# Kernel tuning notes

Measured on AMD Instinct MI355X. Metric: run time of the kernel, lower is better.

The kernel has to match this reference:

```python
import jax, jax.numpy as jnp
import numpy as np
from jax import lax


def _lstm_cell(x, h, c, W_ih, W_hh, b_ih, b_hh):
    # PyTorch LSTMCell math, gate order: input, forget, cell(g), output
    gates = x @ W_ih.T + h @ W_hh.T + b_ih + b_hh  # [B, 4H]
    i, f, g, o = jnp.split(gates, 4, axis=-1)
    i = jax.nn.sigmoid(i)
    f = jax.nn.sigmoid(f)
    g = jnp.tanh(g)
    o = jax.nn.sigmoid(o)
    c_new = f * c + i * g
    h_new = o * jnp.tanh(c_new)
    return h_new, c_new


def setup_inputs() -> dict:
    key = jax.random.key(0)
    ks = jax.random.split(key, 9)
    T, B, D, H = 512, 64, 512, 1024
    s = 0.02  # small init scale to keep recurrence stable
    return {
        "inputs": jax.random.normal(ks[0], (T, B, D), dtype=jnp.float32),
        "W_ih0": jax.random.normal(ks[1], (4 * H, D), dtype=jnp.float32) * s,
        "W_hh0": jax.random.normal(ks[2], (4 * H, H), dtype=jnp.float32) * s,
        "b_ih0": jax.random.normal(ks[3], (4 * H,), dtype=jnp.float32) * s,
        "b_hh0": jax.random.normal(ks[4], (4 * H,), dtype=jnp.float32) * s,
        "W_ih1": jax.random.normal(ks[5], (4 * H, H), dtype=jnp.float32) * s,
        "W_hh1": jax.random.normal(ks[6], (4 * H, H), dtype=jnp.float32) * s,
        "b_ih1": jax.random.normal(ks[7], (4 * H,), dtype=jnp.float32) * s,
        "b_hh1": jax.random.normal(ks[8], (4 * H,), dtype=jnp.float32) * s,
    }


def reference(inputs, W_ih0, W_hh0, b_ih0, b_hh0, W_ih1, W_hh1, b_ih1, b_hh1):
    # 2-layer LSTM over time via lax.scan; dropout=0.0, residual=False.
    T, B, _ = inputs.shape
    H = W_hh0.shape[1]
    z = jnp.zeros((B, H), dtype=inputs.dtype)
    init = (z, z, z, z)  # (h0, c0, h1, c1)

    def step(carry, x_t):
        h0, c0, h1, c1 = carry
        h0, c0 = _lstm_cell(x_t, h0, c0, W_ih0, W_hh0, b_ih0, b_hh0)
        h1, c1 = _lstm_cell(h0, h1, c1, W_ih1, W_hh1, b_ih1, b_hh1)
        return (h0, c0, h1, c1), h1

    (h0, c0, h1, c1), outputs = lax.scan(step, init, inputs)
    # outputs: [T, B, H] from last layer; final states per layer
    return outputs, (h0, c0, h1, c1)
```

## Files before the change

### kernel.cpp

```cpp
#include <hip/hip_runtime.h>
#include <hip/hip_bf16.h>
#include <stdint.h>


#define T_STEPS 512
#define BATCH   64
#define DIN     512
#define HID     1024
#define NBLK    256
#define NTHR    512

typedef __attribute__((ext_vector_type(8)))  short short8;
typedef __attribute__((ext_vector_type(16))) float f32x16;

union U16 { unsigned long long u[2]; short8 v; };

#define OFF_WIH0 ((size_t)0)
#define OFF_WHH0 ((size_t)4194304)
#define OFF_WIH1 ((size_t)12582912)
#define OFF_WHH1 ((size_t)20971520)
#define OFF_XBF  ((size_t)29360128)
#define OFF_H0   ((size_t)62914560)
#define OFF_H1   ((size_t)(OFF_H0 + 262144))
#define OFF_FLG  ((size_t)(OFF_H1 + 262144))

__global__ void cvt_bf16x4(const float4* __restrict__ in,
                           ushort4* __restrict__ out, int n4) {
  int i = blockIdx.x * blockDim.x + threadIdx.x;
  if (i >= n4) return;
  float4 v = in[i];
  __hip_bfloat16 b0 = __float2bfloat16(v.x), b1 = __float2bfloat16(v.y),
                 b2 = __float2bfloat16(v.z), b3 = __float2bfloat16(v.w);
  ushort4 o;
  o.x = *(unsigned short*)&b0; o.y = *(unsigned short*)&b1;
  o.z = *(unsigned short*)&b2; o.w = *(unsigned short*)&b3;
  out[i] = o;
}

__device__ __forceinline__ float sigf(float x) {
  return 1.0f / (1.0f + __expf(-x));
}
__device__ __forceinline__ float tanhfast(float x) {
  return 1.0f - 2.0f / (__expf(2.0f * x) + 1.0f);
}

__launch_bounds__(NTHR, 2)
__global__ void lstm_persist(const __hip_bfloat16* __restrict__ whh0,
                             const __hip_bfloat16* __restrict__ wih0,
                             const __hip_bfloat16* __restrict__ wih1,
                             const __hip_bfloat16* __restrict__ whh1,
                             const __hip_bfloat16* __restrict__ xbf,
                             __hip_bfloat16* h0buf, __hip_bfloat16* h1buf,
                             const float* __restrict__ bih0, const float* __restrict__ bhh0,
                             const float* __restrict__ bih1, const float* __restrict__ bhh1,
                             float* __restrict__ out, unsigned* flags) {
  __shared__ float dump[8][2][32][32];

  const int tid = threadIdx.x;
  const int w   = tid >> 6;
  const int l   = tid & 63;
  const int cu  = blockIdx.x;
  const bool L1cu = (cu >= 128);
  const int q  = L1cu ? (cu - 128) : cu;
  const int jt = q >> 1;
  const int mh = q & 1;

  const int fidx = mh * 128 + (L1cu ? 64 : 0) + jt;

  const int n    = l & 31;
  const int ksub = (l >> 5) * 8;
  const int m    = mh * 32 + n;

  const int erow = tid >> 4;
  const int ehc  = tid & 15;
  const int ecol = jt * 16 + ehc;
  const int em   = mh * 32 + erow;

  float bi, bf_, bg, bo;
  {
    const float* ba = L1cu ? bih1 : bih0;
    const float* bb = L1cu ? bhh1 : bhh0;
    bi  = ba[0 * HID + ecol] + bb[0 * HID + ecol];
    bf_ = ba[1 * HID + ecol] + bb[1 * HID + ecol];
    bg  = ba[2 * HID + ecol] + bb[2 * HID + ecol];
    bo  = ba[3 * HID + ecol] + bb[3 * HID + ecol];
  }
  float cst = 0.0f;

  const int wr0 = ((n >> 4) + 0) * HID + jt * 16 + (n & 15);
  const int wr1 = ((n >> 4) + 2) * HID + jt * 16 + (n & 15);

  short8 w1a[8], w1b[8];
  short8 w2a[8], w2b[8];
  if (!L1cu) {
#pragma unroll
    for (int kk = 0; kk < 8; ++kk) {
      int k0 = (w + 8 * kk) * 16 + ksub;
      w1a[kk] = *(const short8*)(whh0 + (size_t)wr0 * 1024 + k0);
      w1b[kk] = *(const short8*)(whh0 + (size_t)wr1 * 1024 + k0);
    }
#pragma unroll
    for (int kk = 0; kk < 4; ++kk) {
      int k0 = (w + 8 * kk) * 16 + ksub;
      w2a[kk] = *(const short8*)(wih0 + (size_t)wr0 * 512 + k0);
      w2b[kk] = *(const short8*)(wih0 + (size_t)wr1 * 512 + k0);
    }
  } else {
#pragma unroll
    for (int kk = 0; kk < 8; ++kk) {
      int k0 = (w + 8 * kk) * 16 + ksub;
      w1a[kk] = *(const short8*)(wih1 + (size_t)wr0 * 1024 + k0);
      w1b[kk] = *(const short8*)(wih1 + (size_t)wr1 * 1024 + k0);
      w2a[kk] = *(const short8*)(whh1 + (size_t)wr0 * 1024 + k0);
      w2b[kk] = *(const short8*)(whh1 + (size_t)wr1 * 1024 + k0);
    }
  }

  for (int p = 0; p <= T_STEPS; ++p) {
    const bool active  = L1cu ? (p >= 1) : (p < T_STEPS);
    const bool notlast = (p < T_STEPS);
    float h = 0.0f;

    if (active) {
      const int pb = (p + 1) & 1;
      f32x16 acc0, acc1;
#pragma unroll
      for (int r = 0; r < 16; ++r) { acc0[r] = 0.0f; acc1[r] = 0.0f; }

      {
        const __hip_bfloat16* A1e =
            h0buf + (size_t)pb * 65536 + (size_t)m * 1024 + ksub;
        const unsigned long long* A1 = (const unsigned long long*)A1e;
        U16 a1[8];
#pragma unroll
        for (int kk = 0; kk < 8; ++kk) {
          const unsigned long long* pa = A1 + (size_t)(w + 8 * kk) * 4;
          a1[kk].u[0] = __hip_atomic_load(pa,     __ATOMIC_RELAXED, __HIP_MEMORY_SCOPE_AGENT);
          a1[kk].u[1] = __hip_atomic_load(pa + 1, __ATOMIC_RELAXED, __HIP_MEMORY_SCOPE_AGENT);
        }
#pragma unroll
        for (int kk = 0; kk < 8; ++kk) {
          acc0 = __builtin_amdgcn_mfma_f32_32x32x16_bf16(a1[kk].v, w1a[kk], acc0, 0, 0, 0);
          acc1 = __builtin_amdgcn_mfma_f32_32x32x16_bf16(a1[kk].v, w1b[kk], acc1, 0, 0, 0);
        }
      }

      if (!L1cu) {
        const short8* A2 =
            (const short8*)(xbf + ((size_t)p * 64 + m) * 512 + ksub);
        short8 a2[4];
#pragma unroll
        for (int kk = 0; kk < 4; ++kk) a2[kk] = A2[(w + 8 * kk) * 2];
#pragma unroll
        for (int kk = 0; kk < 4; ++kk) {
          acc0 = __builtin_amdgcn_mfma_f32_32x32x16_bf16(a2[kk], w2a[kk], acc0, 0, 0, 0);
          acc1 = __builtin_amdgcn_mfma_f32_32x32x16_bf16(a2[kk], w2b[kk], acc1, 0, 0, 0);
        }
      } else {
        const __hip_bfloat16* A2e =
            h1buf + (size_t)(p & 1) * 65536 + (size_t)m * 1024 + ksub;
        const unsigned long long* A2 = (const unsigned long long*)A2e;
        U16 a2[8];
#pragma unroll
        for (int kk = 0; kk < 8; ++kk) {
          const unsigned long long* pa = A2 + (size_t)(w + 8 * kk) * 4;
          a2[kk].u[0] = __hip_atomic_load(pa,     __ATOMIC_RELAXED, __HIP_MEMORY_SCOPE_AGENT);
          a2[kk].u[1] = __hip_atomic_load(pa + 1, __ATOMIC_RELAXED, __HIP_MEMORY_SCOPE_AGENT);
        }
#pragma unroll
        for (int kk = 0; kk < 8; ++kk) {
          acc0 = __builtin_amdgcn_mfma_f32_32x32x16_bf16(a2[kk].v, w2a[kk], acc0, 0, 0, 0);
          acc1 = __builtin_amdgcn_mfma_f32_32x32x16_bf16(a2[kk].v, w2b[kk], acc1, 0, 0, 0);
        }
      }

      __syncthreads();
#pragma unroll
      for (int r = 0; r < 16; ++r) {
        int row = (r & 3) + 8 * (r >> 2) + 4 * (l >> 5);
        dump[w][0][row][n] = acc0[r];
        dump[w][1][row][n] = acc1[r];
      }
      __syncthreads();

      float gi = bi, gf = bf_, gg = bg, go = bo;
#pragma unroll
      for (int ww = 0; ww < 8; ++ww) {
        gi += dump[ww][0][erow][ehc];
        gf += dump[ww][0][erow][ehc + 16];
        gg += dump[ww][1][erow][ehc];
        go += dump[ww][1][erow][ehc + 16];
      }
      float si = sigf(gi), sf = sigf(gf), so = sigf(go);
      float tg = tanhfast(gg);
      cst = sf * cst + si * tg;
      h = so * tanhfast(cst);

      if (notlast) {
        __hip_bfloat16 hbf = __float2bfloat16(h);
        unsigned hb = *(const unsigned short*)&hbf;
        unsigned pr = __shfl_xor(hb, 1);
        __hip_bfloat16* hdst = L1cu ? (h1buf + (size_t)((p + 1) & 1) * 65536)
                                    : (h0buf + (size_t)(p & 1) * 65536);
        if ((ehc & 1) == 0) {
          unsigned pv = hb | (pr << 16);
          __hip_atomic_store((unsigned*)(hdst + (size_t)em * 1024 + ecol), pv,
                             __ATOMIC_RELAXED, __HIP_MEMORY_SCOPE_AGENT);
        }
      }
    }

    if (notlast) {
      asm volatile("s_waitcnt vmcnt(0)" ::: "memory");
      __syncthreads();
      if (tid == 0)
        __hip_atomic_store(flags + fidx, (unsigned)(p + 1),
                           __ATOMIC_RELAXED, __HIP_MEMORY_SCOPE_AGENT);
    }

    if (active) {
      if (!L1cu) {
        if (p == T_STEPS - 1) {
          out[(size_t)T_STEPS * BATCH * HID + 0 * BATCH * HID + (size_t)em * HID + ecol] = h;
          out[(size_t)T_STEPS * BATCH * HID + 1 * BATCH * HID + (size_t)em * HID + ecol] = cst;
        }
      } else {
        out[((size_t)(p - 1) * BATCH + em) * HID + ecol] = h;
        if (p == T_STEPS) {
          out[(size_t)T_STEPS * BATCH * HID + 2 * BATCH * HID + (size_t)em * HID + ecol] = h;
          out[(size_t)T_STEPS * BATCH * HID + 3 * BATCH * HID + (size_t)em * HID + ecol] = cst;
        }
      }
    }

    if (notlast) {
      if (w == 0) {
        const unsigned tgt = (unsigned)(p + 1);
        const unsigned long long* f64 =
            (const unsigned long long*)(flags + (size_t)mh * 128) + l;
        for (;;) {
          unsigned long long v =
              __hip_atomic_load(f64, __ATOMIC_RELAXED, __HIP_MEMORY_SCOPE_AGENT);
          if (__all(((unsigned)v >= tgt) & ((unsigned)(v >> 32) >= tgt))) break;
          __builtin_amdgcn_s_sleep(1);
        }
      }
      __syncthreads();
    }
  }
}

extern "C" void kernel_launch(void* const* d_in, const int* in_sizes, int n_in,
                              void* d_out, int out_size, void* d_ws, size_t ws_size,
                              hipStream_t stream) {
  const float* x     = (const float*)d_in[0];
  const float* Wih0  = (const float*)d_in[1];
  const float* Whh0  = (const float*)d_in[2];
  const float* b_ih0 = (const float*)d_in[3];
  const float* b_hh0 = (const float*)d_in[4];
  const float* Wih1  = (const float*)d_in[5];
  const float* Whh1  = (const float*)d_in[6];
  const float* b_ih1 = (const float*)d_in[7];
  const float* b_hh1 = (const float*)d_in[8];
  float* out = (float*)d_out;

  char* ws = (char*)d_ws;
  __hip_bfloat16* wih0p = (__hip_bfloat16*)(ws + OFF_WIH0);
  __hip_bfloat16* whh0p = (__hip_bfloat16*)(ws + OFF_WHH0);
  __hip_bfloat16* wih1p = (__hip_bfloat16*)(ws + OFF_WIH1);
  __hip_bfloat16* whh1p = (__hip_bfloat16*)(ws + OFF_WHH1);
  __hip_bfloat16* xbfp  = (__hip_bfloat16*)(ws + OFF_XBF);
  __hip_bfloat16* h0p   = (__hip_bfloat16*)(ws + OFF_H0);
  __hip_bfloat16* h1p   = (__hip_bfloat16*)(ws + OFF_H1);
  unsigned* flg         = (unsigned*)(ws + OFF_FLG);

  hipMemsetAsync(ws + OFF_H0, 0, 262144 * 2 + 1024, stream);

  cvt_bf16x4<<<2048,  256, 0, stream>>>((const float4*)Wih0, (ushort4*)wih0p, 2097152 / 4);
  cvt_bf16x4<<<4096,  256, 0, stream>>>((const float4*)Whh0, (ushort4*)whh0p, 4194304 / 4);
  cvt_bf16x4<<<4096,  256, 0, stream>>>((const float4*)Wih1, (ushort4*)wih1p, 4194304 / 4);
  cvt_bf16x4<<<4096,  256, 0, stream>>>((const float4*)Whh1, (ushort4*)whh1p, 4194304 / 4);
  cvt_bf16x4<<<16384, 256, 0, stream>>>((const float4*)x,    (ushort4*)xbfp, 16777216 / 4);

  void* args[] = { &whh0p, &wih0p, &wih1p, &whh1p, &xbfp, &h0p, &h1p,
                   (void*)&b_ih0, (void*)&b_hh0, (void*)&b_ih1, (void*)&b_hh1,
                   &out, &flg };
  hipLaunchCooperativeKernel((const void*)lstm_persist, dim3(NBLK), dim3(NTHR),
                             args, 0, stream);
}
```

Before: 7.071 ms.

## Replace global flag barrier with per-element tagged hidden-state ring buffers

Drops the per-step grid-wide flag barrier. Each hidden-state element is now stored as a 32-bit word holding a 16-bit step tag and the bf16 value, in an 8-deep ring buffer per layer. Consumers spin on the tags of exactly the words they load, so layer 0 can run up to four steps ahead of layer 1, bounded by a progress counter that layer 1 publishes. This removes the global barrier latency and loosens the lockstep between layers. The cost is twice the hidden-state bytes per load, a byte-permute unpack, and spin loops with iteration caps that could silently read stale data if they time out.

Result: slower. 8.738 ms (+23.6%).

```diff
diff --git a/kernel.cpp b/kernel.cpp
--- a/kernel.cpp
+++ b/kernel.cpp
@@ -13,16 +13,16 @@
 typedef __attribute__((ext_vector_type(8)))  short short8;
 typedef __attribute__((ext_vector_type(16))) float f32x16;
 
-union U16 { unsigned long long u[2]; short8 v; };
+union S8U { unsigned u[4]; short8 v; };
 
 #define OFF_WIH0 ((size_t)0)
 #define OFF_WHH0 ((size_t)4194304)
 #define OFF_WIH1 ((size_t)12582912)
 #define OFF_WHH1 ((size_t)20971520)
 #define OFF_XBF  ((size_t)29360128)
-#define OFF_H0   ((size_t)62914560)
-#define OFF_H1   ((size_t)(OFF_H0 + 262144))
-#define OFF_FLG  ((size_t)(OFF_H1 + 262144))
+#define OFF_H0R  ((size_t)62914560)
+#define OFF_H1R  ((size_t)(OFF_H0R + 2097152))
+#define OFF_PRG  ((size_t)(OFF_H1R + 2097152))
 
 __global__ void cvt_bf16x4(const float4* __restrict__ in,
                            ushort4* __restrict__ out, int n4) {
@@ -44,16 +44,60 @@
   return 1.0f - 2.0f / (__expf(2.0f * x) + 1.0f);
 }
 
+__device__ __forceinline__ bool tag_ok4(uint4 q, unsigned short t16) {
+  return ((unsigned short)q.x == t16) & ((unsigned short)q.y == t16) &
+         ((unsigned short)q.z == t16) & ((unsigned short)q.w == t16);
+}
+
+__device__ __forceinline__ void load_tagged8(const unsigned* sb, int w,
+                                             unsigned tg, short8 frag[8]) {
+  const unsigned short t16 = (unsigned short)tg;
+  uint4 wa[8], wb[8];
+#pragma unroll
+  for (int kk = 0; kk < 8; ++kk) {
+    const unsigned* pk = sb + (size_t)(w + 8 * kk) * 16;
+    asm volatile("global_load_dwordx4 %0, %1, off" : "=v"(wa[kk]) : "v"(pk) : "memory");
+    asm volatile("global_load_dwordx4 %0, %1, off" : "=v"(wb[kk]) : "v"(pk + 4) : "memory");
+  }
+  asm volatile("s_waitcnt vmcnt(0)" ::: "memory");
+#pragma unroll
+  for (int kk = 0; kk < 8; ++kk) {
+    const unsigned* pk = sb + (size_t)(w + 8 * kk) * 16;
+    int tries = 0;
+    while (!__all(tag_ok4(wa[kk], t16))) {
+      if (++tries > (1 << 22)) break;
+      __builtin_amdgcn_s_sleep(2);
+      asm volatile("global_load_dwordx4 %0, %1, off sc0 sc1"
+                   : "=v"(wa[kk]) : "v"(pk) : "memory");
+      asm volatile("s_waitcnt vmcnt(0)" ::: "memory");
+    }
+    tries = 0;
+    while (!__all(tag_ok4(wb[kk], t16))) {
+      if (++tries > (1 << 22)) break;
+      __builtin_amdgcn_s_sleep(2);
+      asm volatile("global_load_dwordx4 %0, %1, off sc0 sc1"
+                   : "=v"(wb[kk]) : "v"(pk + 4) : "memory");
+      asm volatile("s_waitcnt vmcnt(0)" ::: "memory");
+    }
+    S8U f;
+    f.u[0] = __builtin_amdgcn_perm(wa[kk].y, wa[kk].x, 0x07060302);
+    f.u[1] = __builtin_amdgcn_perm(wa[kk].w, wa[kk].z, 0x07060302);
+    f.u[2] = __builtin_amdgcn_perm(wb[kk].y, wb[kk].x, 0x07060302);
+    f.u[3] = __builtin_amdgcn_perm(wb[kk].w, wb[kk].z, 0x07060302);
+    frag[kk] = f.v;
+  }
+}
+
 __launch_bounds__(NTHR, 2)
 __global__ void lstm_persist(const __hip_bfloat16* __restrict__ whh0,
                              const __hip_bfloat16* __restrict__ wih0,
                              const __hip_bfloat16* __restrict__ wih1,
                              const __hip_bfloat16* __restrict__ whh1,
                              const __hip_bfloat16* __restrict__ xbf,
-                             __hip_bfloat16* h0buf, __hip_bfloat16* h1buf,
+                             unsigned* h0r, unsigned* h1r, unsigned* prog,
                              const float* __restrict__ bih0, const float* __restrict__ bhh0,
                              const float* __restrict__ bih1, const float* __restrict__ bhh1,
-                             float* __restrict__ out, unsigned* flags) {
+                             float* __restrict__ out) {
   __shared__ float dump[8][2][32][32];
 
   const int tid = threadIdx.x;
@@ -65,8 +109,6 @@
   const int jt = q >> 1;
   const int mh = q & 1;
 
-  const int fidx = mh * 128 + (L1cu ? 64 : 0) + jt;
-
   const int n    = l & 31;
   const int ksub = (l >> 5) * 8;
   const int m    = mh * 32 + n;
@@ -116,62 +158,33 @@
     }
   }
 
-  for (int p = 0; p <= T_STEPS; ++p) {
-    const bool active  = L1cu ? (p >= 1) : (p < T_STEPS);
-    const bool notlast = (p < T_STEPS);
-    float h = 0.0f;
-
-    if (active) {
-      const int pb = (p + 1) & 1;
+  if (!L1cu) {
+    for (int p = 0; p < T_STEPS; ++p) {
+      int progv = (int)__hip_atomic_load(prog + mh * 64 + l,
+                                         __ATOMIC_RELAXED, __HIP_MEMORY_SCOPE_AGENT);
+
       f32x16 acc0, acc1;
 #pragma unroll
       for (int r = 0; r < 16; ++r) { acc0[r] = 0.0f; acc1[r] = 0.0f; }
 
-      {
-        const __hip_bfloat16* A1e =
-            h0buf + (size_t)pb * 65536 + (size_t)m * 1024 + ksub;
-        const unsigned long long* A1 = (const unsigned long long*)A1e;
-        U16 a1[8];
-#pragma unroll
-        for (int kk = 0; kk < 8; ++kk) {
-          const unsigned long long* pa = A1 + (size_t)(w + 8 * kk) * 4;
-          a1[kk].u[0] = __hip_atomic_load(pa,     __ATOMIC_RELAXED, __HIP_MEMORY_SCOPE_AGENT);
-          a1[kk].u[1] = __hip_atomic_load(pa + 1, __ATOMIC_RELAXED, __HIP_MEMORY_SCOPE_AGENT);
-        }
-#pragma unroll
-        for (int kk = 0; kk < 8; ++kk) {
-          acc0 = __builtin_amdgcn_mfma_f32_32x32x16_bf16(a1[kk].v, w1a[kk], acc0, 0, 0, 0);
-          acc1 = __builtin_amdgcn_mfma_f32_32x32x16_bf16(a1[kk].v, w1b[kk], acc1, 0, 0, 0);
-        }
-      }
-
-      if (!L1cu) {
-        const short8* A2 =
-            (const short8*)(xbf + ((size_t)p * 64 + m) * 512 + ksub);
-        short8 a2[4];
-#pragma unroll
-        for (int kk = 0; kk < 4; ++kk) a2[kk] = A2[(w + 8 * kk) * 2];
-#pragma unroll
-        for (int kk = 0; kk < 4; ++kk) {
-          acc0 = __builtin_amdgcn_mfma_f32_32x32x16_bf16(a2[kk], w2a[kk], acc0, 0, 0, 0);
-          acc1 = __builtin_amdgcn_mfma_f32_32x32x16_bf16(a2[kk], w2b[kk], acc1, 0, 0, 0);
-        }
-      } else {
-        const __hip_bfloat16* A2e =
-            h1buf + (size_t)(p & 1) * 65536 + (size_t)m * 1024 + ksub;
-        const unsigned long long* A2 = (const unsigned long long*)A2e;
-        U16 a2[8];
-#pragma unroll
-        for (int kk = 0; kk < 8; ++kk) {
-          const unsigned long long* pa = A2 + (size_t)(w + 8 * kk) * 4;
-          a2[kk].u[0] = __hip_atomic_load(pa,     __ATOMIC_RELAXED, __HIP_MEMORY_SCOPE_AGENT);
-          a2[kk].u[1] = __hip_atomic_load(pa + 1, __ATOMIC_RELAXED, __HIP_MEMORY_SCOPE_AGENT);
-        }
-#pragma unroll
-        for (int kk = 0; kk < 8; ++kk) {
-          acc0 = __builtin_amdgcn_mfma_f32_32x32x16_bf16(a2[kk].v, w2a[kk], acc0, 0, 0, 0);
-          acc1 = __builtin_amdgcn_mfma_f32_32x32x16_bf16(a2[kk].v, w2b[kk], acc1, 0, 0, 0);
-        }
+      short8 a1[8];
+      load_tagged8(h0r + (size_t)((p + 7) & 7) * 65536 + (size_t)m * 1024 + ksub,
+                   w, (unsigned)p, a1);
+
+      const short8* A2 = (const short8*)(xbf + ((size_t)p * 64 + m) * 512 + ksub);
+      short8 a2[4];
+#pragma unroll
+      for (int kk = 0; kk < 4; ++kk) a2[kk] = A2[(w + 8 * kk) * 2];
+
+#pragma unroll
+      for (int kk = 0; kk < 8; ++kk) {
+        acc0 = __builtin_amdgcn_mfma_f32_32x32x16_bf16(a1[kk], w1a[kk], acc0, 0, 0, 0);
+        acc1 = __builtin_amdgcn_mfma_f32_32x32x16_bf16(a1[kk], w1b[kk], acc1, 0, 0, 0);
+      }
+#pragma unroll
+      for (int kk = 0; kk < 4; ++kk) {
+        acc0 = __builtin_amdgcn_mfma_f32_32x32x16_bf16(a2[kk], w2a[kk], acc0, 0, 0, 0);
+        acc1 = __builtin_amdgcn_mfma_f32_32x32x16_bf16(a2[kk], w2b[kk], acc1, 0, 0, 0);
       }
 
       __syncthreads();
@@ -194,58 +207,98 @@
       float si = sigf(gi), sf = sigf(gf), so = sigf(go);
       float tg = tanhfast(gg);
       cst = sf * cst + si * tg;
-      h = so * tanhfast(cst);
-
-      if (notlast) {
+      float h = so * tanhfast(cst);
+
+      {
+        const int need = p - 4;
+        int tries = 0;
+        while (!__all(progv >= need)) {
+          if (++tries > (1 << 22)) break;
+          __builtin_amdgcn_s_sleep(8);
+          progv = (int)__hip_atomic_load(prog + mh * 64 + l,
+                                         __ATOMIC_RELAXED, __HIP_MEMORY_SCOPE_AGENT);
+        }
+      }
+
+      {
         __hip_bfloat16 hbf = __float2bfloat16(h);
-        unsigned hb = *(const unsigned short*)&hbf;
-        unsigned pr = __shfl_xor(hb, 1);
-        __hip_bfloat16* hdst = L1cu ? (h1buf + (size_t)((p + 1) & 1) * 65536)
-                                    : (h0buf + (size_t)(p & 1) * 65536);
-        if ((ehc & 1) == 0) {
-          unsigned pv = hb | (pr << 16);
-          __hip_atomic_store((unsigned*)(hdst + (size_t)em * 1024 + ecol), pv,
-                             __ATOMIC_RELAXED, __HIP_MEMORY_SCOPE_AGENT);
-        }
-      }
-    }
-
-    if (notlast) {
-      asm volatile("s_waitcnt vmcnt(0)" ::: "memory");
+        unsigned word = ((unsigned)(p + 1) & 0xFFFFu) |
+                        ((unsigned)*(const unsigned short*)&hbf << 16);
+        __hip_atomic_store(h0r + (size_t)(p & 7) * 65536 + (size_t)em * 1024 + ecol,
+                           word, __ATOMIC_RELAXED, __HIP_MEMORY_SCOPE_AGENT);
+      }
+
+      if (p == T_STEPS - 1) {
+        out[(size_t)T_STEPS * BATCH * HID + 0 * BATCH * HID + (size_t)em * HID + ecol] = h;
+        out[(size_t)T_STEPS * BATCH * HID + 1 * BATCH * HID + (size_t)em * HID + ecol] = cst;
+      }
+    }
+  } else {
+    for (int p = 1; p <= T_STEPS; ++p) {
+      f32x16 acc0, acc1;
+#pragma unroll
+      for (int r = 0; r < 16; ++r) { acc0[r] = 0.0f; acc1[r] = 0.0f; }
+
+      short8 a1[8];
+      load_tagged8(h0r + (size_t)((p + 7) & 7) * 65536 + (size_t)m * 1024 + ksub,
+                   w, (unsigned)p, a1);
+#pragma unroll
+      for (int kk = 0; kk < 8; ++kk) {
+        acc0 = __builtin_amdgcn_mfma_f32_32x32x16_bf16(a1[kk], w1a[kk], acc0, 0, 0, 0);
+        acc1 = __builtin_amdgcn_mfma_f32_32x32x16_bf16(a1[kk], w1b[kk], acc1, 0, 0, 0);
+      }
+
+      short8 a2[8];
+      {
+        unsigned tg1 = (p == 1) ? 0u : (unsigned)p;
+        load_tagged8(h1r + (size_t)((p + 7) & 7) * 65536 + (size_t)m * 1024 + ksub,
+                     w, tg1, a2);
+      }
+#pragma unroll
+      for (int kk = 0; kk < 8; ++kk) {
+        acc0 = __builtin_amdgcn_mfma_f32_32x32x16_bf16(a2[kk], w2a[kk], acc0, 0, 0, 0);
+        acc1 = __builtin_amdgcn_mfma_f32_32x32x16_bf16(a2[kk], w2b[kk], acc1, 0, 0, 0);
+      }
+
       __syncthreads();
+#pragma unroll
+      for (int r = 0; r < 16; ++r) {
+        int row = (r & 3) + 8 * (r >> 2) + 4 * (l >> 5);
+        dump[w][0][row][n] = acc0[r];
+        dump[w][1][row][n] = acc1[r];
+      }
+      __syncthreads();
+
+      float gi = bi, gf = bf_, gg = bg, go = bo;
+#pragma unroll
+      for (int ww = 0; ww < 8; ++ww) {
+        gi += dump[ww][0][erow][ehc];
+        gf += dump[ww][0][erow][ehc + 16];
+        gg += dump[ww][1][erow][ehc];
+        go += dump[ww][1][erow][ehc + 16];
+      }
+      float si = sigf(gi), sf = sigf(gf), so = sigf(go);
+      float tg = tanhfast(gg);
+      cst = sf * cst + si * tg;
+      float h = so * tanhfast(cst);
+
+      if (p <= T_STEPS - 1) {
+        __hip_bfloat16 hbf = __float2bfloat16(h);
+        unsigned word = ((unsigned)(p + 1) & 0xFFFFu) |
+                        ((unsigned)*(const unsigned short*)&hbf << 16);
+        __hip_atomic_store(h1r + (size_t)(p & 7) * 65536 + (size_t)em * 1024 + ecol,
+                           word, __ATOMIC_RELAXED, __HIP_MEMORY_SCOPE_AGENT);
+      }
+
       if (tid == 0)
-        __hip_atomic_store(flags + fidx, (unsigned)(p + 1),
+        __hip_atomic_store(prog + mh * 64 + jt, (unsigned)p,
                            __ATOMIC_RELAXED, __HIP_MEMORY_SCOPE_AGENT);
-    }
-
-    if (active) {
-      if (!L1cu) {
-        if (p == T_STEPS - 1) {
-          out[(size_t)T_STEPS * BATCH * HID + 0 * BATCH * HID + (size_t)em * HID + ecol] = h;
-          out[(size_t)T_STEPS * BATCH * HID + 1 * BATCH * HID + (size_t)em * HID + ecol] = cst;
-        }
-      } else {
-        out[((size_t)(p - 1) * BATCH + em) * HID + ecol] = h;
-        if (p == T_STEPS) {
-          out[(size_t)T_STEPS * BATCH * HID + 2 * BATCH * HID + (size_t)em * HID + ecol] = h;
-          out[(size_t)T_STEPS * BATCH * HID + 3 * BATCH * HID + (size_t)em * HID + ecol] = cst;
-        }
-      }
-    }
-
-    if (notlast) {
-      if (w == 0) {
-        const unsigned tgt = (unsigned)(p + 1);
-        const unsigned long long* f64 =
-            (const unsigned long long*)(flags + (size_t)mh * 128) + l;
-        for (;;) {
-          unsigned long long v =
-              __hip_atomic_load(f64, __ATOMIC_RELAXED, __HIP_MEMORY_SCOPE_AGENT);
-          if (__all(((unsigned)v >= tgt) & ((unsigned)(v >> 32) >= tgt))) break;
-          __builtin_amdgcn_s_sleep(1);
-        }
-      }
-      __syncthreads();
+
+      out[((size_t)(p - 1) * BATCH + em) * HID + ecol] = h;
+      if (p == T_STEPS) {
+        out[(size_t)T_STEPS * BATCH * HID + 2 * BATCH * HID + (size_t)em * HID + ecol] = h;
+        out[(size_t)T_STEPS * BATCH * HID + 3 * BATCH * HID + (size_t)em * HID + ecol] = cst;
+      }
     }
   }
 }
@@ -270,11 +323,11 @@
   __hip_bfloat16* wih1p = (__hip_bfloat16*)(ws + OFF_WIH1);
   __hip_bfloat16* whh1p = (__hip_bfloat16*)(ws + OFF_WHH1);
   __hip_bfloat16* xbfp  = (__hip_bfloat16*)(ws + OFF_XBF);
-  __hip_bfloat16* h0p   = (__hip_bfloat16*)(ws + OFF_H0);
-  __hip_bfloat16* h1p   = (__hip_bfloat16*)(ws + OFF_H1);
-  unsigned* flg         = (unsigned*)(ws + OFF_FLG);
-
-  hipMemsetAsync(ws + OFF_H0, 0, 262144 * 2 + 1024, stream);
+  unsigned* h0rp        = (unsigned*)(ws + OFF_H0R);
+  unsigned* h1rp        = (unsigned*)(ws + OFF_H1R);
+  unsigned* prgp        = (unsigned*)(ws + OFF_PRG);
+
+  hipMemsetAsync(ws + OFF_H0R, 0, 2097152 * 2 + 1024, stream);
 
   cvt_bf16x4<<<2048,  256, 0, stream>>>((const float4*)Wih0, (ushort4*)wih0p, 2097152 / 4);
   cvt_bf16x4<<<4096,  256, 0, stream>>>((const float4*)Whh0, (ushort4*)whh0p, 4194304 / 4);
@@ -282,9 +335,9 @@
   cvt_bf16x4<<<4096,  256, 0, stream>>>((const float4*)Whh1, (ushort4*)whh1p, 4194304 / 4);
   cvt_bf16x4<<<16384, 256, 0, stream>>>((const float4*)x,    (ushort4*)xbfp, 16777216 / 4);
 
-  void* args[] = { &whh0p, &wih0p, &wih1p, &whh1p, &xbfp, &h0p, &h1p,
+  void* args[] = { &whh0p, &wih0p, &wih1p, &whh1p, &xbfp, &h0rp, &h1rp, &prgp,
                    (void*)&b_ih0, (void*)&b_hh0, (void*)&b_ih1, (void*)&b_hh1,
-                   &out, &flg };
+                   &out };
   hipLaunchCooperativeKernel((const void*)lstm_persist, dim3(NBLK), dim3(NTHR),
                              args, 0, stream);
 }
```
